# Performance work log

Hardware: AMD Instinct MI355X
Metric: run time of the kernel (lower is better)

Reference implementation:

```python
import jax, jax.numpy as jnp
import numpy as np
import math

B, S, HID = 2, 2048, 512
NH, NKV, HD = 8, 2, 256
ROT = 64          # partial_rotary_factor 0.25 * head_dim 256
ROPE_THETA = 10000000.0
EPS = 1e-6


def _rms_norm(x, w):
    # zero-centered RMSNorm: x / rms * (1 + w)
    rms = jnp.sqrt(jnp.mean(x * x, axis=-1, keepdims=True) + EPS)
    return x / rms * (1.0 + w)


def _partial_rope(x, cos, sin):
    # x: [B,S,H,HD]; cos/sin: [S, ROT//2]
    xr = x[..., :ROT].reshape(*x.shape[:-1], ROT // 2, 2)
    a, b = xr[..., 0], xr[..., 1]
    c = cos[None, :, None, :]
    s = sin[None, :, None, :]
    rot = jnp.stack([a * c - b * s, a * s + b * c], axis=-1).reshape(*x.shape[:-1], ROT)
    return jnp.concatenate([rot, x[..., ROT:]], axis=-1)


def setup_inputs() -> dict:
    key = jax.random.key(0)
    ks = jax.random.split(key, 6)
    x = jax.random.normal(ks[0], (B, S, HID), dtype=jnp.float32)
    # real RoPE frequencies
    inv_freq = 1.0 / (ROPE_THETA ** (np.arange(0, ROT, 2, dtype=np.float32) / ROT))
    t = np.arange(S, dtype=np.float32)
    angles = np.outer(t, inv_freq)  # [S, ROT//2]
    cos = jnp.asarray(np.cos(angles), dtype=jnp.float32)
    sin = jnp.asarray(np.sin(angles), dtype=jnp.float32)
    # additive causal mask [S,S]
    mask = jnp.where(jnp.tril(jnp.ones((S, S), dtype=bool)), 0.0, -1e9).astype(jnp.float32)
    sc = 0.02
    wq = jax.random.normal(ks[1], (HID, NH * HD), dtype=jnp.float32) * sc
    wk = jax.random.normal(ks[2], (HID, NKV * HD), dtype=jnp.float32) * sc
    wv = jax.random.normal(ks[3], (HID, NKV * HD), dtype=jnp.float32) * sc
    wo = jax.random.normal(ks[4], (NH * HD, HID), dtype=jnp.float32) * sc
    q_norm_w = jnp.zeros((HD,), dtype=jnp.float32)
    k_norm_w = jnp.zeros((HD,), dtype=jnp.float32)
    return {"x": x, "cos": cos, "sin": sin, "mask": mask,
            "wq": wq, "wk": wk, "wv": wv, "wo": wo,
            "q_norm_w": q_norm_w, "k_norm_w": k_norm_w}


def reference(x, cos, sin, mask, wq, wk, wv, wo, q_norm_w, k_norm_w):
    b, s, _ = x.shape
    groups = NH // NKV
    q = (x @ wq).reshape(b, s, NH, HD)
    k = (x @ wk).reshape(b, s, NKV, HD)
    v = (x @ wv).reshape(b, s, NKV, HD)
    q = _partial_rope(_rms_norm(q, q_norm_w), cos, sin)
    k = _partial_rope(_rms_norm(k, k_norm_w), cos, sin)
    # GQA: broadcast kv heads to NH
    k = jnp.repeat(k, groups, axis=2)  # [b,s,NH,HD]
    v = jnp.repeat(v, groups, axis=2)
    scale = math.sqrt(HD)
    scores = jnp.einsum('bqhd,bkhd->bhqk', q, k) / scale
    scores = scores + mask[None, None, :, :]
    attn = jax.nn.softmax(scores, axis=-1)
    out = jnp.einsum('bhqk,bkhd->bqhd', attn, v).reshape(b, s, NH * HD)
    return out @ wo
```

## Files before the change

### kernel.cpp

```cpp
#include <hip/hip_runtime.h>

#define S_LEN 2048
#define NHQ 8
#define NKV 2
#define HD 256
#define KVB 32

typedef __attribute__((ext_vector_type(8))) short bf16x8;
typedef __attribute__((ext_vector_type(4))) short bf16x4;
typedef __attribute__((ext_vector_type(4))) float f32x4;
typedef __attribute__((ext_vector_type(16))) float f32x16;
typedef __attribute__((ext_vector_type(4))) unsigned u32x4;

__device__ __forceinline__ short f2bf(float f) {
    unsigned u = __builtin_bit_cast(unsigned, f);
    u += 0x7FFFu + ((u >> 16) & 1u);
    return (short)(u >> 16);
}
__device__ __forceinline__ float bf2f(short s) {
    unsigned u = ((unsigned)(unsigned short)s) << 16;
    return __builtin_bit_cast(float, u);
}
__device__ __forceinline__ unsigned cvtpk(float a, float b) {
    unsigned r;
    asm("v_cvt_pk_bf16_f32 %0, %1, %2" : "=v"(r) : "v"(a), "v"(b));
    return r;
}
__device__ __forceinline__ void gload16(const short* g, short* l) {
    __builtin_amdgcn_global_load_lds((const __attribute__((address_space(1))) unsigned*)g,
                                     (__attribute__((address_space(3))) unsigned*)l, 16, 0, 0);
}
__device__ __forceinline__ float bperm(int srclane, float v) {
    return __builtin_bit_cast(float,
        __builtin_amdgcn_ds_bpermute(srclane * 4, __builtin_bit_cast(int, v)));
}

__global__ __launch_bounds__(256) void cvt_kernel(const float* __restrict__ in,
                                                  short* __restrict__ out, int n) {
    int i = (blockIdx.x * 256 + threadIdx.x) * 4;
    if (i + 3 < n) {
        float4 f = *(const float4*)(in + i);
        bf16x4 o;
        o[0] = f2bf(f.x); o[1] = f2bf(f.y); o[2] = f2bf(f.z); o[3] = f2bf(f.w);
        *(bf16x4*)(out + i) = o;
    }
}

__global__ __launch_bounds__(256) void wt_kernel(const float* __restrict__ in,
                                                 short* __restrict__ out,
                                                 int K, int N) {
    __shared__ short tile[64][72];
    int n0 = blockIdx.x * 64, k0 = blockIdx.y * 64;
    int t = threadIdx.x;
    #pragma unroll
    for (int i = 0; i < 16; i++) {
        int flat = i * 256 + t; int r = flat >> 6, c = flat & 63;
        tile[r][c] = f2bf(in[(long)(k0 + r) * N + n0 + c]);
    }
    __syncthreads();
    #pragma unroll
    for (int i = 0; i < 16; i++) {
        int flat = i * 256 + t; int r = flat >> 6, c = flat & 63;
        out[(long)(n0 + r) * K + k0 + c] = tile[c][r];
    }
}

template<int BN, int WRITE_BF16>
__global__ __launch_bounds__(256) void gemm_bt(const short* __restrict__ A,
                                               const short* __restrict__ Bt,
                                               void* __restrict__ Cv,
                                               int M, int N, int K) {
    constexpr int NI = BN / 32;
    __shared__ short As[128 * 32];
    __shared__ short Bs[BN * 32];
    const int t = threadIdx.x;
    const int lane = t & 63, w = t >> 6;
    const int lr = lane & 15, lg = lane >> 4;
    const int m0 = blockIdx.y * 128, n0 = blockIdx.x * BN;
    const int wm = (w >> 1) * 64, wn = (w & 1) * (BN / 2);

    f32x4 acc[4][NI];
    #pragma unroll
    for (int i = 0; i < 4; i++)
        #pragma unroll
        for (int j = 0; j < NI; j++) acc[i][j] = (f32x4){0.f, 0.f, 0.f, 0.f};

    for (int k0 = 0; k0 < K; k0 += 32) {
        __syncthreads();
        #pragma unroll
        for (int r = 0; r < 2; r++) {
            int sbase = r * 2048 + w * 512;
            int srow = (sbase + lane * 8) >> 5, scol = (sbase + lane * 8) & 31;
            gload16(A + (long)(m0 + srow) * K + k0 + scol, &As[sbase]);
        }
        #pragma unroll
        for (int r = 0; r < BN / 64; r++) {
            int sbase = r * 2048 + w * 512;
            int srow = (sbase + lane * 8) >> 5, scol = (sbase + lane * 8) & 31;
            gload16(Bt + (long)(n0 + srow) * K + k0 + scol, &Bs[sbase]);
        }
        __syncthreads();
        bf16x8 af[4], bfr[NI];
        #pragma unroll
        for (int mi = 0; mi < 4; mi++)
            af[mi] = *(const bf16x8*)&As[(wm + mi * 16 + lr) * 32 + lg * 8];
        #pragma unroll
        for (int ni = 0; ni < NI; ni++)
            bfr[ni] = *(const bf16x8*)&Bs[(wn + ni * 16 + lr) * 32 + lg * 8];
        #pragma unroll
        for (int mi = 0; mi < 4; mi++)
            #pragma unroll
            for (int ni = 0; ni < NI; ni++)
                acc[mi][ni] = __builtin_amdgcn_mfma_f32_16x16x32_bf16(af[mi], bfr[ni], acc[mi][ni], 0, 0, 0);
    }
    #pragma unroll
    for (int mi = 0; mi < 4; mi++)
    #pragma unroll
    for (int ni = 0; ni < NI; ni++)
    #pragma unroll
    for (int r = 0; r < 4; r++) {
        long row = m0 + wm + mi * 16 + lg * 4 + r;
        long col = n0 + wn + ni * 16 + lr;
        float v = acc[mi][ni][r];
        if (WRITE_BF16) ((short*)Cv)[row * N + col] = f2bf(v);
        else            ((float*)Cv)[row * N + col] = v;
    }
}

__global__ __launch_bounds__(256) void norm_rope_kernel(
    const short* __restrict__ in, short* __restrict__ out,
    const float* __restrict__ w, const float* __restrict__ cosb,
    const float* __restrict__ sinb, int H, long ldin, long cofs,
    long ob, long oh, long os, float scale) {
    int vec = blockIdx.x * 4 + (threadIdx.x >> 6);
    int lane = threadIdx.x & 63;
    int token = vec / H, head = vec % H;
    int b = token / S_LEN, s = token % S_LEN;

    bf16x4 xv = *(const bf16x4*)(in + (long)token * ldin + cofs + head * 256 + lane * 4);
    float x0 = bf2f(xv[0]), x1 = bf2f(xv[1]), x2 = bf2f(xv[2]), x3 = bf2f(xv[3]);
    float ss = x0 * x0 + x1 * x1 + x2 * x2 + x3 * x3;
    #pragma unroll
    for (int m = 1; m < 64; m <<= 1) ss += __shfl_xor(ss, m);
    float inv = rsqrtf(ss * (1.f / 256.f) + 1e-6f);

    float4 wv = *(const float4*)(w + lane * 4);
    float y0 = x0 * inv * (1.f + wv.x);
    float y1 = x1 * inv * (1.f + wv.y);
    float y2 = x2 * inv * (1.f + wv.z);
    float y3 = x3 * inv * (1.f + wv.w);

    if (lane < 16) {
        float2 c = *(const float2*)&cosb[s * 32 + lane * 2];
        float2 sn = *(const float2*)&sinb[s * 32 + lane * 2];
        float a0 = y0 * c.x - y1 * sn.x, b0 = y0 * sn.x + y1 * c.x;
        float a1 = y2 * c.y - y3 * sn.y, b1 = y2 * sn.y + y3 * c.y;
        y0 = a0; y1 = b0; y2 = a1; y3 = b1;
    }
    y0 *= scale; y1 *= scale; y2 *= scale; y3 *= scale;
    long oidx = (long)b * ob + (long)head * oh + (long)s * os + lane * 4;
    bf16x4 o; o[0] = f2bf(y0); o[1] = f2bf(y1); o[2] = f2bf(y2); o[3] = f2bf(y3);
    *(bf16x4*)(out + oidx) = o;
}

__global__ __launch_bounds__(256) void transpose_v_kernel(const short* __restrict__ C,
                                                          short* __restrict__ vr) {
    __shared__ short tile[64][65];
    int s0 = blockIdx.x * 64, d0 = blockIdx.y * 64;
    int bkv = blockIdx.z; int b = bkv >> 1, kv = bkv & 1;
    int t = threadIdx.x;
    #pragma unroll
    for (int i = 0; i < 16; i++) {
        int flat = i * 256 + t; int si = flat >> 6, di = flat & 63;
        tile[si][di] = C[(long)(b * S_LEN + s0 + si) * 3072 + 2560 + kv * 256 + d0 + di];
    }
    __syncthreads();
    #pragma unroll
    for (int i = 0; i < 16; i++) {
        int flat = i * 256 + t; int di = flat >> 6, si = flat & 63;
        vr[(long)(bkv * 256 + d0 + di) * S_LEN + s0 + si] = tile[si][di];
    }
}

__global__ __launch_bounds__(256, 2) void flash_kernel(const short* __restrict__ Q,
                                                       const short* __restrict__ Kt,
                                                       const short* __restrict__ Vt,
                                                       short* __restrict__ O) {
    __shared__ __align__(16) char smem[66048];

    int idx = blockIdx.x;
    int xcd = idx & 7, slot = idx >> 3;
    int bh = xcd * 2 + (slot & 1);
    int j  = 31 - (slot >> 1);
    int h = bh & 7, b = bh >> 3;
    int kv = h >> 2;
    int t = threadIdx.x, lane = t & 63, w = t >> 6;
    int g = w >> 1, p = w & 1;
    int ln = lane & 31, hi = lane >> 5;
    int q0 = j * 64 + g * 32;
    int qg = q0 + ln;

    const short* Kb = Kt + (long)(b * NKV + kv) * S_LEN * HD;
    const short* Vb = Vt + (long)(b * NKV + kv) * HD * S_LEN;

    bf16x8 qf[16];
    {
        const short* qrow = Q + ((long)(b * S_LEN + qg) * NHQ + h) * HD + hi * 8;
        #pragma unroll
        for (int dc = 0; dc < 16; dc++) qf[dc] = *(const bf16x8*)&qrow[dc * 16];
    }

    f32x16 acc[8];
    #pragma unroll
    for (int i = 0; i < 8; i++)
        #pragma unroll
        for (int jj = 0; jj < 16; jj++) acc[i][jj] = 0.f;
    float m = -1e30f, l = 0.f;

    auto stage = [&](int ph2) {
        #pragma unroll
        for (int pp = 0; pp < 2; pp++) {
            int k0s = (2 * ph2 + pp) * KVB;
            short* Ktile = (short*)(smem + pp * 16384);
            short* Vtile = (short*)(smem + 32768 + pp * 16384);
            #pragma unroll
            for (int c = 0; c < 4; c++) {
                int o = c * 4096 + w * 1024 + lane * 16;
                int key = o >> 9, db = o & 511;
                gload16(Kb + (long)(k0s + key) * HD + ((db ^ ((key & 7) << 4)) >> 1),
                        Ktile + (c * 4096 + w * 1024) / 2);
                int d = o >> 6, kb = o & 63;
                gload16(Vb + (long)d * S_LEN + k0s + ((kb ^ ((d & 6) << 3)) >> 1),
                        Vtile + (c * 4096 + w * 1024) / 2);
            }
        }
    };

    auto compute = [&](int k0) {
        const char* Ks = (const char*)smem + p * 16384;
        const char* Vs = (const char*)smem + 32768 + p * 16384;
        f32x16 sA, sB;
        #pragma unroll
        for (int r = 0; r < 16; r++) { sA[r] = 0.f; sB[r] = 0.f; }
        __builtin_amdgcn_s_setprio(1);
        #pragma unroll
        for (int dc = 0; dc < 16; dc += 2) {
            int kb0 = (dc * 32 + hi * 16) ^ ((ln & 7) << 4);
            int kb1 = ((dc + 1) * 32 + hi * 16) ^ ((ln & 7) << 4);
            bf16x8 kf0 = *(const bf16x8*)(Ks + ln * 512 + kb0);
            bf16x8 kf1 = *(const bf16x8*)(Ks + ln * 512 + kb1);
            sA = __builtin_amdgcn_mfma_f32_32x32x16_bf16(kf0, qf[dc],     sA, 0, 0, 0);
            sB = __builtin_amdgcn_mfma_f32_32x32x16_bf16(kf1, qf[dc + 1], sB, 0, 0, 0);
        }
        __builtin_amdgcn_s_setprio(0);
        f32x16 s;
        #pragma unroll
        for (int r = 0; r < 16; r++) s[r] = sA[r] + sB[r];

        if (k0 + KVB - 1 > q0) {
            #pragma unroll
            for (int r = 0; r < 16; r++) {
                int key_g = k0 + (r & 3) + 8 * (r >> 2) + 4 * hi;
                if (key_g > qg) s[r] = -1e30f;
            }
        }
        float mt = s[0];
        #pragma unroll
        for (int r = 1; r < 16; r++) mt = fmaxf(mt, s[r]);
        mt = fmaxf(mt, __shfl_xor(mt, 32));
        float mn = m;
        if (!__all(mt <= m + 8.f)) {
            mn = fmaxf(m, mt);
            float f = __expf(m - mn);
            m = mn;
            float fr[16];
            #pragma unroll
            for (int r = 0; r < 16; r++)
                fr[r] = bperm((r & 3) + 8 * (r >> 2) + 4 * hi, f);
            #pragma unroll
            for (int i = 0; i < 8; i++)
                #pragma unroll
                for (int r = 0; r < 16; r++) acc[i][r] *= fr[r];
            l *= f;
        }
        float pr[16], ps = 0.f;
        #pragma unroll
        for (int r = 0; r < 16; r++) { pr[r] = __expf(s[r] - mn); ps += pr[r]; }
        ps += __shfl_xor(ps, 32);
        l += ps;

        unsigned pw[8];
        #pragma unroll
        for (int kc = 0; kc < 2; kc++) {
            unsigned X = cvtpk(pr[kc * 8 + 0], pr[kc * 8 + 1]);
            unsigned Y = cvtpk(pr[kc * 8 + 4], pr[kc * 8 + 5]);
            unsigned Z = cvtpk(pr[kc * 8 + 2], pr[kc * 8 + 3]);
            unsigned W = cvtpk(pr[kc * 8 + 6], pr[kc * 8 + 7]);
            asm volatile("v_permlane32_swap_b32 %0, %1" : "+v"(X), "+v"(Y));
            asm volatile("v_permlane32_swap_b32 %0, %1" : "+v"(Z), "+v"(W));
            pw[kc * 4 + 0] = X; pw[kc * 4 + 1] = Z;
            pw[kc * 4 + 2] = Y; pw[kc * 4 + 3] = W;
        }
        u32x4 w0v = {pw[0], pw[1], pw[2], pw[3]};
        u32x4 w1v = {pw[4], pw[5], pw[6], pw[7]};
        bf16x8 pa0 = __builtin_bit_cast(bf16x8, w0v);
        bf16x8 pa1 = __builtin_bit_cast(bf16x8, w1v);

        __builtin_amdgcn_s_setprio(1);
        #pragma unroll
        for (int db = 0; db < 8; db++) {
            int drow = db * 32 + ln;
            int sw = (drow & 6) << 3;
            bf16x8 vf0 = *(const bf16x8*)(Vs + drow * 64 + ((hi * 16) ^ sw));
            bf16x8 vf1 = *(const bf16x8*)(Vs + drow * 64 + ((32 + hi * 16) ^ sw));
            acc[db] = __builtin_amdgcn_mfma_f32_32x32x16_bf16(pa0, vf0, acc[db], 0, 0, 0);
            acc[db] = __builtin_amdgcn_mfma_f32_32x32x16_bf16(pa1, vf1, acc[db], 0, 0, 0);
        }
        __builtin_amdgcn_s_setprio(0);
    };

    stage(0);
    for (int ph = 0; ph <= j; ph++) {
        asm volatile("s_waitcnt vmcnt(0)" ::: "memory");
        __builtin_amdgcn_s_barrier();
        int k0 = (2 * ph + p) * KVB;
        if (k0 <= q0 + 31) compute(k0);
        __builtin_amdgcn_s_barrier();
        if (ph < j) stage(ph + 1);
        __builtin_amdgcn_sched_barrier(0);
    }

    float* accb = (float*)smem;
    float* mlb  = (float*)(smem + 65536);
    if (p == 1) {
        #pragma unroll
        for (int db = 0; db < 8; db++)
            #pragma unroll
            for (int r = 0; r < 16; r++)
                accb[g * 8192 + (db * 16 + r) * 64 + hi * 32 + ln] = acc[db][r];
        if (hi == 0) { mlb[g * 32 + ln] = m; mlb[64 + g * 32 + ln] = l; }
    }
    __syncthreads();
    if (p == 0) {
        float m1 = mlb[g * 32 + ln], l1 = mlb[64 + g * 32 + ln];
        float M  = fmaxf(m, m1);
        float f0 = __expf(m - M), f1 = __expf(m1 - M);
        float lt = l * f0 + l1 * f1;
        float w0 = f0 / lt, w1 = f1 / lt;
        float fr0[16], fr1[16];
        #pragma unroll
        for (int r = 0; r < 16; r++) {
            int crow = (r & 3) + 8 * (r >> 2) + 4 * hi;
            fr0[r] = bperm(crow, w0);
            fr1[r] = bperm(crow, w1);
        }
        #pragma unroll
        for (int db = 0; db < 8; db++)
            #pragma unroll
            for (int r = 0; r < 16; r++) {
                float a1 = accb[g * 8192 + (db * 16 + r) * 64 + hi * 32 + ln];
                int qrow = q0 + (r & 3) + 8 * (r >> 2) + 4 * hi;
                O[(long)(b * S_LEN + qrow) * 2048 + h * HD + db * 32 + ln] =
                    f2bf(acc[db][r] * fr0[r] + a1 * fr1[r]);
            }
    }
}

extern "C" void kernel_launch(void* const* d_in, const int* in_sizes, int n_in,
                              void* d_out, int out_size, void* d_ws, size_t ws_size,
                              hipStream_t stream) {
    const float* x    = (const float*)d_in[0];
    const float* cosb = (const float*)d_in[1];
    const float* sinb = (const float*)d_in[2];
    const float* wq   = (const float*)d_in[4];
    const float* wk   = (const float*)d_in[5];
    const float* wv   = (const float*)d_in[6];
    const float* wo   = (const float*)d_in[7];
    const float* qnw  = (const float*)d_in[8];
    const float* knw  = (const float*)d_in[9];
    float* out = (float*)d_out;

    char* ws = (char*)d_ws;
    short* xb   = (short*)(ws + 0);
    short* wfus = (short*)(ws + 4194304);
    short* wot  = (short*)(ws + 7340032);
    short* C    = (short*)(ws + 9437184);
    short* ao   = (short*)(ws + 9437184);
    short* qro  = (short*)(ws + 34603008);
    short* kr   = (short*)(ws + 51380224);
    short* vr   = (short*)(ws + 55574528);

    cvt_kernel<<<2048, 256, 0, stream>>>(x, xb, 2097152);
    wt_kernel<<<dim3(32, 8), 256, 0, stream>>>(wq, wfus,              512, 2048);
    wt_kernel<<<dim3(8, 8),  256, 0, stream>>>(wk, wfus + 2048 * 512, 512, 512);
    wt_kernel<<<dim3(8, 8),  256, 0, stream>>>(wv, wfus + 2560 * 512, 512, 512);
    wt_kernel<<<dim3(8, 32), 256, 0, stream>>>(wo, wot, 2048, 512);

    gemm_bt<128, 1><<<dim3(24, 32), 256, 0, stream>>>(xb, wfus, C, 4096, 3072, 512);

    norm_rope_kernel<<<8192, 256, 0, stream>>>(C, qro, qnw, cosb, sinb, 8,
                                               3072L, 0L, 4194304L, 256L, 2048L, 0.0625f);
    norm_rope_kernel<<<2048, 256, 0, stream>>>(C, kr, knw, cosb, sinb, 2,
                                               3072L, 2048L, 1048576L, 524288L, 256L, 1.0f);
    transpose_v_kernel<<<dim3(32, 4, 4), 256, 0, stream>>>(C, vr);

    flash_kernel<<<512, 256, 0, stream>>>(qro, kr, vr, ao);

    gemm_bt<64, 0><<<dim3(8, 32), 256, 0, stream>>>(ao, wot, out, 4096, 512, 2048);
}
```

Measured before the change: 199.9 us.

## Fuse Q norm+RoPE into flash kernel and split K/V staging pipeline

Removes the separate Q RMSNorm+RoPE kernel. The flash kernel now reads raw Q from the fused projection output and applies the norm, rotary and scale in registers while the first K/V tiles load. The K and V loads are split into separate stages with partial vmcnt waits, so the next K tile loads during softmax and PV, and V loads during the next QK. The block-to-tile mapping is also changed to pair long and short causal rows across the two grid halves. This adds barriers per iteration and more register pressure.

```diff
diff --git a/kernel.cpp b/kernel.cpp
--- a/kernel.cpp
+++ b/kernel.cpp
@@ -182,16 +182,21 @@
     }
 }
 
-__global__ __launch_bounds__(256, 2) void flash_kernel(const short* __restrict__ Q,
+__global__ __launch_bounds__(256, 2) void flash_kernel(const short* __restrict__ Cq,
                                                        const short* __restrict__ Kt,
                                                        const short* __restrict__ Vt,
-                                                       short* __restrict__ O) {
+                                                       short* __restrict__ O,
+                                                       const float* __restrict__ qnw,
+                                                       const float* __restrict__ cosb,
+                                                       const float* __restrict__ sinb) {
     __shared__ __align__(16) char smem[66048];
 
     int idx = blockIdx.x;
-    int xcd = idx & 7, slot = idx >> 3;
+    int half = idx >> 8, rm = idx & 255;
+    int xcd = rm & 7, slot = rm >> 3;
     int bh = xcd * 2 + (slot & 1);
-    int j  = 31 - (slot >> 1);
+    int jj = slot >> 1;
+    int j  = half ? jj : (31 - jj);
     int h = bh & 7, b = bh >> 3;
     int kv = h >> 2;
     int t = threadIdx.x, lane = t & 63, w = t >> 6;
@@ -203,32 +208,28 @@
     const short* Kb = Kt + (long)(b * NKV + kv) * S_LEN * HD;
     const short* Vb = Vt + (long)(b * NKV + kv) * HD * S_LEN;
 
-    bf16x8 qf[16];
-    {
-        const short* qrow = Q + ((long)(b * S_LEN + qg) * NHQ + h) * HD + hi * 8;
-        #pragma unroll
-        for (int dc = 0; dc < 16; dc++) qf[dc] = *(const bf16x8*)&qrow[dc * 16];
-    }
-
-    f32x16 acc[8];
-    #pragma unroll
-    for (int i = 0; i < 8; i++)
-        #pragma unroll
-        for (int jj = 0; jj < 16; jj++) acc[i][jj] = 0.f;
-    float m = -1e30f, l = 0.f;
-
-    auto stage = [&](int ph2) {
+    auto stageK = [&](int ph2) {
         #pragma unroll
         for (int pp = 0; pp < 2; pp++) {
             int k0s = (2 * ph2 + pp) * KVB;
             short* Ktile = (short*)(smem + pp * 16384);
-            short* Vtile = (short*)(smem + 32768 + pp * 16384);
             #pragma unroll
             for (int c = 0; c < 4; c++) {
                 int o = c * 4096 + w * 1024 + lane * 16;
                 int key = o >> 9, db = o & 511;
                 gload16(Kb + (long)(k0s + key) * HD + ((db ^ ((key & 7) << 4)) >> 1),
                         Ktile + (c * 4096 + w * 1024) / 2);
+            }
+        }
+    };
+    auto stageV = [&](int ph2) {
+        #pragma unroll
+        for (int pp = 0; pp < 2; pp++) {
+            int k0s = (2 * ph2 + pp) * KVB;
+            short* Vtile = (short*)(smem + 32768 + pp * 16384);
+            #pragma unroll
+            for (int c = 0; c < 4; c++) {
+                int o = c * 4096 + w * 1024 + lane * 16;
                 int d = o >> 6, kb = o & 63;
                 gload16(Vb + (long)d * S_LEN + k0s + ((kb ^ ((d & 6) << 3)) >> 1),
                         Vtile + (c * 4096 + w * 1024) / 2);
@@ -236,98 +237,159 @@
         }
     };
 
-    auto compute = [&](int k0) {
-        const char* Ks = (const char*)smem + p * 16384;
-        const char* Vs = (const char*)smem + 32768 + p * 16384;
-        f32x16 sA, sB;
-        #pragma unroll
-        for (int r = 0; r < 16; r++) { sA[r] = 0.f; sB[r] = 0.f; }
-        __builtin_amdgcn_s_setprio(1);
-        #pragma unroll
-        for (int dc = 0; dc < 16; dc += 2) {
-            int kb0 = (dc * 32 + hi * 16) ^ ((ln & 7) << 4);
-            int kb1 = ((dc + 1) * 32 + hi * 16) ^ ((ln & 7) << 4);
-            bf16x8 kf0 = *(const bf16x8*)(Ks + ln * 512 + kb0);
-            bf16x8 kf1 = *(const bf16x8*)(Ks + ln * 512 + kb1);
-            sA = __builtin_amdgcn_mfma_f32_32x32x16_bf16(kf0, qf[dc],     sA, 0, 0, 0);
-            sB = __builtin_amdgcn_mfma_f32_32x32x16_bf16(kf1, qf[dc + 1], sB, 0, 0, 0);
-        }
-        __builtin_amdgcn_s_setprio(0);
-        f32x16 s;
-        #pragma unroll
-        for (int r = 0; r < 16; r++) s[r] = sA[r] + sB[r];
-
-        if (k0 + KVB - 1 > q0) {
-            #pragma unroll
-            for (int r = 0; r < 16; r++) {
-                int key_g = k0 + (r & 3) + 8 * (r >> 2) + 4 * hi;
-                if (key_g > qg) s[r] = -1e30f;
-            }
-        }
-        float mt = s[0];
-        #pragma unroll
-        for (int r = 1; r < 16; r++) mt = fmaxf(mt, s[r]);
-        mt = fmaxf(mt, __shfl_xor(mt, 32));
-        float mn = m;
-        if (!__all(mt <= m + 8.f)) {
-            mn = fmaxf(m, mt);
-            float f = __expf(m - mn);
-            m = mn;
-            float fr[16];
-            #pragma unroll
-            for (int r = 0; r < 16; r++)
-                fr[r] = bperm((r & 3) + 8 * (r >> 2) + 4 * hi, f);
-            #pragma unroll
-            for (int i = 0; i < 8; i++)
-                #pragma unroll
-                for (int r = 0; r < 16; r++) acc[i][r] *= fr[r];
-            l *= f;
-        }
-        float pr[16], ps = 0.f;
-        #pragma unroll
-        for (int r = 0; r < 16; r++) { pr[r] = __expf(s[r] - mn); ps += pr[r]; }
-        ps += __shfl_xor(ps, 32);
-        l += ps;
-
-        unsigned pw[8];
-        #pragma unroll
-        for (int kc = 0; kc < 2; kc++) {
-            unsigned X = cvtpk(pr[kc * 8 + 0], pr[kc * 8 + 1]);
-            unsigned Y = cvtpk(pr[kc * 8 + 4], pr[kc * 8 + 5]);
-            unsigned Z = cvtpk(pr[kc * 8 + 2], pr[kc * 8 + 3]);
-            unsigned W = cvtpk(pr[kc * 8 + 6], pr[kc * 8 + 7]);
-            asm volatile("v_permlane32_swap_b32 %0, %1" : "+v"(X), "+v"(Y));
-            asm volatile("v_permlane32_swap_b32 %0, %1" : "+v"(Z), "+v"(W));
-            pw[kc * 4 + 0] = X; pw[kc * 4 + 1] = Z;
-            pw[kc * 4 + 2] = Y; pw[kc * 4 + 3] = W;
-        }
-        u32x4 w0v = {pw[0], pw[1], pw[2], pw[3]};
-        u32x4 w1v = {pw[4], pw[5], pw[6], pw[7]};
-        bf16x8 pa0 = __builtin_bit_cast(bf16x8, w0v);
-        bf16x8 pa1 = __builtin_bit_cast(bf16x8, w1v);
-
-        __builtin_amdgcn_s_setprio(1);
-        #pragma unroll
-        for (int db = 0; db < 8; db++) {
-            int drow = db * 32 + ln;
-            int sw = (drow & 6) << 3;
-            bf16x8 vf0 = *(const bf16x8*)(Vs + drow * 64 + ((hi * 16) ^ sw));
-            bf16x8 vf1 = *(const bf16x8*)(Vs + drow * 64 + ((32 + hi * 16) ^ sw));
-            acc[db] = __builtin_amdgcn_mfma_f32_32x32x16_bf16(pa0, vf0, acc[db], 0, 0, 0);
-            acc[db] = __builtin_amdgcn_mfma_f32_32x32x16_bf16(pa1, vf1, acc[db], 0, 0, 0);
-        }
-        __builtin_amdgcn_s_setprio(0);
-    };
-
-    stage(0);
+    stageK(0); stageV(0);
+
+    bf16x8 qf[16];
+    {
+        const short* qrow = Cq + (long)(b * S_LEN + qg) * 3072 + h * 256 + hi * 8;
+        #pragma unroll
+        for (int dc = 0; dc < 16; dc++) qf[dc] = *(const bf16x8*)&qrow[dc * 16];
+        float ss = 0.f;
+        #pragma unroll
+        for (int dc = 0; dc < 16; dc++)
+            #pragma unroll
+            for (int e = 0; e < 8; e++) { float v = bf2f(qf[dc][e]); ss += v * v; }
+        ss += __shfl_xor(ss, 32);
+        float inv = rsqrtf(ss * (1.f / 256.f) + 1e-6f);
+        #pragma unroll
+        for (int dc = 0; dc < 16; dc++) {
+            float y[8];
+            float4 w0 = *(const float4*)&qnw[dc * 16 + hi * 8];
+            float4 w1 = *(const float4*)&qnw[dc * 16 + hi * 8 + 4];
+            y[0] = bf2f(qf[dc][0]) * inv * (1.f + w0.x);
+            y[1] = bf2f(qf[dc][1]) * inv * (1.f + w0.y);
+            y[2] = bf2f(qf[dc][2]) * inv * (1.f + w0.z);
+            y[3] = bf2f(qf[dc][3]) * inv * (1.f + w0.w);
+            y[4] = bf2f(qf[dc][4]) * inv * (1.f + w1.x);
+            y[5] = bf2f(qf[dc][5]) * inv * (1.f + w1.y);
+            y[6] = bf2f(qf[dc][6]) * inv * (1.f + w1.z);
+            y[7] = bf2f(qf[dc][7]) * inv * (1.f + w1.w);
+            if (dc < 4) {
+                float4 c4 = *(const float4*)&cosb[qg * 32 + dc * 8 + hi * 4];
+                float4 s4 = *(const float4*)&sinb[qg * 32 + dc * 8 + hi * 4];
+                float a, bb;
+                a = y[0]; bb = y[1]; y[0] = a * c4.x - bb * s4.x; y[1] = a * s4.x + bb * c4.x;
+                a = y[2]; bb = y[3]; y[2] = a * c4.y - bb * s4.y; y[3] = a * s4.y + bb * c4.y;
+                a = y[4]; bb = y[5]; y[4] = a * c4.z - bb * s4.z; y[5] = a * s4.z + bb * c4.z;
+                a = y[6]; bb = y[7]; y[6] = a * c4.w - bb * s4.w; y[7] = a * s4.w + bb * c4.w;
+            }
+            bf16x8 o;
+            #pragma unroll
+            for (int e = 0; e < 8; e++) o[e] = f2bf(y[e] * 0.0625f);
+            qf[dc] = o;
+        }
+    }
+
+    f32x16 acc[8];
+    #pragma unroll
+    for (int i = 0; i < 8; i++)
+        #pragma unroll
+        for (int r = 0; r < 16; r++) acc[i][r] = 0.f;
+    float m = -1e30f, l = 0.f;
+
     for (int ph = 0; ph <= j; ph++) {
-        asm volatile("s_waitcnt vmcnt(0)" ::: "memory");
+        const bool last = (ph == j);
+        asm volatile("s_waitcnt vmcnt(8)" ::: "memory");
         __builtin_amdgcn_s_barrier();
         int k0 = (2 * ph + p) * KVB;
-        if (k0 <= q0 + 31) compute(k0);
+        bool act = (k0 <= q0 + 31);
+
+        f32x16 s;
+        if (act) {
+            const char* Ks = (const char*)smem + p * 16384;
+            f32x16 sA, sB;
+            #pragma unroll
+            for (int r = 0; r < 16; r++) { sA[r] = 0.f; sB[r] = 0.f; }
+            __builtin_amdgcn_s_setprio(1);
+            #pragma unroll
+            for (int dc = 0; dc < 16; dc += 2) {
+                int kb0 = (dc * 32 + hi * 16) ^ ((ln & 7) << 4);
+                int kb1 = ((dc + 1) * 32 + hi * 16) ^ ((ln & 7) << 4);
+                bf16x8 kf0 = *(const bf16x8*)(Ks + ln * 512 + kb0);
+                bf16x8 kf1 = *(const bf16x8*)(Ks + ln * 512 + kb1);
+                sA = __builtin_amdgcn_mfma_f32_32x32x16_bf16(kf0, qf[dc],     sA, 0, 0, 0);
+                sB = __builtin_amdgcn_mfma_f32_32x32x16_bf16(kf1, qf[dc + 1], sB, 0, 0, 0);
+            }
+            __builtin_amdgcn_s_setprio(0);
+            #pragma unroll
+            for (int r = 0; r < 16; r++) s[r] = sA[r] + sB[r];
+        }
         __builtin_amdgcn_s_barrier();
-        if (ph < j) stage(ph + 1);
+        if (!last) stageK(ph + 1);
         __builtin_amdgcn_sched_barrier(0);
+
+        bf16x8 pa0, pa1;
+        if (act) {
+            if (k0 + KVB - 1 > q0) {
+                #pragma unroll
+                for (int r = 0; r < 16; r++) {
+                    int key_g = k0 + (r & 3) + 8 * (r >> 2) + 4 * hi;
+                    if (key_g > qg) s[r] = -1e30f;
+                }
+            }
+            float mt = s[0];
+            #pragma unroll
+            for (int r = 1; r < 16; r++) mt = fmaxf(mt, s[r]);
+            mt = fmaxf(mt, __shfl_xor(mt, 32));
+            float mn = m;
+            if (!__all(mt <= m + 8.f)) {
+                mn = fmaxf(m, mt);
+                float f = __expf(m - mn);
+                m = mn;
+                float fr[16];
+                #pragma unroll
+                for (int r = 0; r < 16; r++)
+                    fr[r] = bperm((r & 3) + 8 * (r >> 2) + 4 * hi, f);
+                #pragma unroll
+                for (int i = 0; i < 8; i++)
+                    #pragma unroll
+                    for (int r = 0; r < 16; r++) acc[i][r] *= fr[r];
+                l *= f;
+            }
+            float pr[16], ps = 0.f;
+            #pragma unroll
+            for (int r = 0; r < 16; r++) { pr[r] = __expf(s[r] - mn); ps += pr[r]; }
+            ps += __shfl_xor(ps, 32);
+            l += ps;
+
+            unsigned pw[8];
+            #pragma unroll
+            for (int kc = 0; kc < 2; kc++) {
+                unsigned X = cvtpk(pr[kc * 8 + 0], pr[kc * 8 + 1]);
+                unsigned Y = cvtpk(pr[kc * 8 + 4], pr[kc * 8 + 5]);
+                unsigned Z = cvtpk(pr[kc * 8 + 2], pr[kc * 8 + 3]);
+                unsigned W = cvtpk(pr[kc * 8 + 6], pr[kc * 8 + 7]);
+                asm volatile("v_permlane32_swap_b32 %0, %1" : "+v"(X), "+v"(Y));
+                asm volatile("v_permlane32_swap_b32 %0, %1" : "+v"(Z), "+v"(W));
+                pw[kc * 4 + 0] = X; pw[kc * 4 + 1] = Z;
+                pw[kc * 4 + 2] = Y; pw[kc * 4 + 3] = W;
+            }
+            u32x4 w0v = {pw[0], pw[1], pw[2], pw[3]};
+            u32x4 w1v = {pw[4], pw[5], pw[6], pw[7]};
+            pa0 = __builtin_bit_cast(bf16x8, w0v);
+            pa1 = __builtin_bit_cast(bf16x8, w1v);
+        }
+
+        if (last) { asm volatile("s_waitcnt vmcnt(0)" ::: "memory"); }
+        else      { asm volatile("s_waitcnt vmcnt(8)" ::: "memory"); }
+        __builtin_amdgcn_s_barrier();
+
+        if (act) {
+            const char* Vs = (const char*)smem + 32768 + p * 16384;
+            __builtin_amdgcn_s_setprio(1);
+            #pragma unroll
+            for (int db = 0; db < 8; db++) {
+                int drow = db * 32 + ln;
+                int sw = (drow & 6) << 3;
+                bf16x8 vf0 = *(const bf16x8*)(Vs + drow * 64 + ((hi * 16) ^ sw));
+                bf16x8 vf1 = *(const bf16x8*)(Vs + drow * 64 + ((32 + hi * 16) ^ sw));
+                acc[db] = __builtin_amdgcn_mfma_f32_32x32x16_bf16(pa0, vf0, acc[db], 0, 0, 0);
+                acc[db] = __builtin_amdgcn_mfma_f32_32x32x16_bf16(pa1, vf1, acc[db], 0, 0, 0);
+            }
+            __builtin_amdgcn_s_setprio(0);
+        }
+        __builtin_amdgcn_s_barrier();
+        if (!last) stageV(ph + 1);
     }
 
     float* accb = (float*)smem;
@@ -385,8 +447,7 @@
     short* wfus = (short*)(ws + 4194304);
     short* wot  = (short*)(ws + 7340032);
     short* C    = (short*)(ws + 9437184);
-    short* ao   = (short*)(ws + 9437184);
-    short* qro  = (short*)(ws + 34603008);
+    short* ao   = (short*)(ws + 34603008);
     short* kr   = (short*)(ws + 51380224);
     short* vr   = (short*)(ws + 55574528);
 
@@ -398,13 +459,11 @@
 
     gemm_bt<128, 1><<<dim3(24, 32), 256, 0, stream>>>(xb, wfus, C, 4096, 3072, 512);
 
-    norm_rope_kernel<<<8192, 256, 0, stream>>>(C, qro, qnw, cosb, sinb, 8,
-                                               3072L, 0L, 4194304L, 256L, 2048L, 0.0625f);
     norm_rope_kernel<<<2048, 256, 0, stream>>>(C, kr, knw, cosb, sinb, 2,
                                                3072L, 2048L, 1048576L, 524288L, 256L, 1.0f);
     transpose_v_kernel<<<dim3(32, 4, 4), 256, 0, stream>>>(C, vr);
 
-    flash_kernel<<<512, 256, 0, stream>>>(qro, kr, vr, ao);
+    flash_kernel<<<512, 256, 0, stream>>>(C, kr, vr, ao, qnw, cosb, sinb);
 
     gemm_bt<64, 0><<<dim3(8, 32), 256, 0, stream>>>(ao, wot, out, 4096, 512, 2048);
 }
```

Measured after the change: 201.8 us. Within noise of the previous version (+0.9%).

## Split K and V staging to overlap next-tile loads with softmax and PV

Applied to the files above, without the earlier changes.

Separates the shared-memory staging of K and V tiles so the next K tile is loaded right after QK^T, while softmax and PV run, and the next V tile is loaded after PV. Waits become partial (vmcnt(8)) instead of draining all loads, and Q fragment loads are issued after the first stage is launched. The aim is to hide global-load latency behind compute, at the cost of an extra barrier per iteration and reliance on a precise in-flight load count.

```diff
diff --git a/kernel.cpp b/kernel.cpp
--- a/kernel.cpp
+++ b/kernel.cpp
@@ -203,32 +203,28 @@
     const short* Kb = Kt + (long)(b * NKV + kv) * S_LEN * HD;
     const short* Vb = Vt + (long)(b * NKV + kv) * HD * S_LEN;
 
-    bf16x8 qf[16];
-    {
-        const short* qrow = Q + ((long)(b * S_LEN + qg) * NHQ + h) * HD + hi * 8;
-        #pragma unroll
-        for (int dc = 0; dc < 16; dc++) qf[dc] = *(const bf16x8*)&qrow[dc * 16];
-    }
-
-    f32x16 acc[8];
-    #pragma unroll
-    for (int i = 0; i < 8; i++)
-        #pragma unroll
-        for (int jj = 0; jj < 16; jj++) acc[i][jj] = 0.f;
-    float m = -1e30f, l = 0.f;
-
-    auto stage = [&](int ph2) {
+    auto stageK = [&](int ph2) {
         #pragma unroll
         for (int pp = 0; pp < 2; pp++) {
             int k0s = (2 * ph2 + pp) * KVB;
             short* Ktile = (short*)(smem + pp * 16384);
-            short* Vtile = (short*)(smem + 32768 + pp * 16384);
             #pragma unroll
             for (int c = 0; c < 4; c++) {
                 int o = c * 4096 + w * 1024 + lane * 16;
                 int key = o >> 9, db = o & 511;
                 gload16(Kb + (long)(k0s + key) * HD + ((db ^ ((key & 7) << 4)) >> 1),
                         Ktile + (c * 4096 + w * 1024) / 2);
+            }
+        }
+    };
+    auto stageV = [&](int ph2) {
+        #pragma unroll
+        for (int pp = 0; pp < 2; pp++) {
+            int k0s = (2 * ph2 + pp) * KVB;
+            short* Vtile = (short*)(smem + 32768 + pp * 16384);
+            #pragma unroll
+            for (int c = 0; c < 4; c++) {
+                int o = c * 4096 + w * 1024 + lane * 16;
                 int d = o >> 6, kb = o & 63;
                 gload16(Vb + (long)d * S_LEN + k0s + ((kb ^ ((d & 6) << 3)) >> 1),
                         Vtile + (c * 4096 + w * 1024) / 2);
@@ -236,98 +232,125 @@
         }
     };
 
-    auto compute = [&](int k0) {
-        const char* Ks = (const char*)smem + p * 16384;
-        const char* Vs = (const char*)smem + 32768 + p * 16384;
-        f32x16 sA, sB;
-        #pragma unroll
-        for (int r = 0; r < 16; r++) { sA[r] = 0.f; sB[r] = 0.f; }
-        __builtin_amdgcn_s_setprio(1);
-        #pragma unroll
-        for (int dc = 0; dc < 16; dc += 2) {
-            int kb0 = (dc * 32 + hi * 16) ^ ((ln & 7) << 4);
-            int kb1 = ((dc + 1) * 32 + hi * 16) ^ ((ln & 7) << 4);
-            bf16x8 kf0 = *(const bf16x8*)(Ks + ln * 512 + kb0);
-            bf16x8 kf1 = *(const bf16x8*)(Ks + ln * 512 + kb1);
-            sA = __builtin_amdgcn_mfma_f32_32x32x16_bf16(kf0, qf[dc],     sA, 0, 0, 0);
-            sB = __builtin_amdgcn_mfma_f32_32x32x16_bf16(kf1, qf[dc + 1], sB, 0, 0, 0);
-        }
-        __builtin_amdgcn_s_setprio(0);
-        f32x16 s;
-        #pragma unroll
-        for (int r = 0; r < 16; r++) s[r] = sA[r] + sB[r];
-
-        if (k0 + KVB - 1 > q0) {
-            #pragma unroll
-            for (int r = 0; r < 16; r++) {
-                int key_g = k0 + (r & 3) + 8 * (r >> 2) + 4 * hi;
-                if (key_g > qg) s[r] = -1e30f;
-            }
-        }
-        float mt = s[0];
-        #pragma unroll
-        for (int r = 1; r < 16; r++) mt = fmaxf(mt, s[r]);
-        mt = fmaxf(mt, __shfl_xor(mt, 32));
-        float mn = m;
-        if (!__all(mt <= m + 8.f)) {
-            mn = fmaxf(m, mt);
-            float f = __expf(m - mn);
-            m = mn;
-            float fr[16];
-            #pragma unroll
-            for (int r = 0; r < 16; r++)
-                fr[r] = bperm((r & 3) + 8 * (r >> 2) + 4 * hi, f);
-            #pragma unroll
-            for (int i = 0; i < 8; i++)
-                #pragma unroll
-                for (int r = 0; r < 16; r++) acc[i][r] *= fr[r];
-            l *= f;
-        }
-        float pr[16], ps = 0.f;
-        #pragma unroll
-        for (int r = 0; r < 16; r++) { pr[r] = __expf(s[r] - mn); ps += pr[r]; }
-        ps += __shfl_xor(ps, 32);
-        l += ps;
-
-        unsigned pw[8];
-        #pragma unroll
-        for (int kc = 0; kc < 2; kc++) {
-            unsigned X = cvtpk(pr[kc * 8 + 0], pr[kc * 8 + 1]);
-            unsigned Y = cvtpk(pr[kc * 8 + 4], pr[kc * 8 + 5]);
-            unsigned Z = cvtpk(pr[kc * 8 + 2], pr[kc * 8 + 3]);
-            unsigned W = cvtpk(pr[kc * 8 + 6], pr[kc * 8 + 7]);
-            asm volatile("v_permlane32_swap_b32 %0, %1" : "+v"(X), "+v"(Y));
-            asm volatile("v_permlane32_swap_b32 %0, %1" : "+v"(Z), "+v"(W));
-            pw[kc * 4 + 0] = X; pw[kc * 4 + 1] = Z;
-            pw[kc * 4 + 2] = Y; pw[kc * 4 + 3] = W;
-        }
-        u32x4 w0v = {pw[0], pw[1], pw[2], pw[3]};
-        u32x4 w1v = {pw[4], pw[5], pw[6], pw[7]};
-        bf16x8 pa0 = __builtin_bit_cast(bf16x8, w0v);
-        bf16x8 pa1 = __builtin_bit_cast(bf16x8, w1v);
-
-        __builtin_amdgcn_s_setprio(1);
-        #pragma unroll
-        for (int db = 0; db < 8; db++) {
-            int drow = db * 32 + ln;
-            int sw = (drow & 6) << 3;
-            bf16x8 vf0 = *(const bf16x8*)(Vs + drow * 64 + ((hi * 16) ^ sw));
-            bf16x8 vf1 = *(const bf16x8*)(Vs + drow * 64 + ((32 + hi * 16) ^ sw));
-            acc[db] = __builtin_amdgcn_mfma_f32_32x32x16_bf16(pa0, vf0, acc[db], 0, 0, 0);
-            acc[db] = __builtin_amdgcn_mfma_f32_32x32x16_bf16(pa1, vf1, acc[db], 0, 0, 0);
-        }
-        __builtin_amdgcn_s_setprio(0);
-    };
-
-    stage(0);
+    stageK(0); stageV(0);
+
+    bf16x8 qf[16];
+    {
+        const short* qrow = Q + ((long)(b * S_LEN + qg) * NHQ + h) * HD + hi * 8;
+        #pragma unroll
+        for (int dc = 0; dc < 16; dc++) qf[dc] = *(const bf16x8*)&qrow[dc * 16];
+    }
+
+    f32x16 acc[8];
+    #pragma unroll
+    for (int i = 0; i < 8; i++)
+        #pragma unroll
+        for (int r = 0; r < 16; r++) acc[i][r] = 0.f;
+    float m = -1e30f, l = 0.f;
+
     for (int ph = 0; ph <= j; ph++) {
-        asm volatile("s_waitcnt vmcnt(0)" ::: "memory");
+        const bool last = (ph == j);
+        asm volatile("s_waitcnt vmcnt(8)" ::: "memory");
         __builtin_amdgcn_s_barrier();
         int k0 = (2 * ph + p) * KVB;
-        if (k0 <= q0 + 31) compute(k0);
+        bool act = (k0 <= q0 + 31);
+
+        f32x16 s;
+        if (act) {
+            const char* Ks = (const char*)smem + p * 16384;
+            f32x16 sA, sB;
+            #pragma unroll
+            for (int r = 0; r < 16; r++) { sA[r] = 0.f; sB[r] = 0.f; }
+            __builtin_amdgcn_s_setprio(1);
+            #pragma unroll
+            for (int dc = 0; dc < 16; dc += 2) {
+                int kb0 = (dc * 32 + hi * 16) ^ ((ln & 7) << 4);
+                int kb1 = ((dc + 1) * 32 + hi * 16) ^ ((ln & 7) << 4);
+                bf16x8 kf0 = *(const bf16x8*)(Ks + ln * 512 + kb0);
+                bf16x8 kf1 = *(const bf16x8*)(Ks + ln * 512 + kb1);
+                sA = __builtin_amdgcn_mfma_f32_32x32x16_bf16(kf0, qf[dc],     sA, 0, 0, 0);
+                sB = __builtin_amdgcn_mfma_f32_32x32x16_bf16(kf1, qf[dc + 1], sB, 0, 0, 0);
+            }
+            __builtin_amdgcn_s_setprio(0);
+            #pragma unroll
+            for (int r = 0; r < 16; r++) s[r] = sA[r] + sB[r];
+        }
         __builtin_amdgcn_s_barrier();
-        if (ph < j) stage(ph + 1);
+        if (!last) stageK(ph + 1);
         __builtin_amdgcn_sched_barrier(0);
+
+        bf16x8 pa0, pa1;
+        if (act) {
+            if (k0 + KVB - 1 > q0) {
+                #pragma unroll
+                for (int r = 0; r < 16; r++) {
+                    int key_g = k0 + (r & 3) + 8 * (r >> 2) + 4 * hi;
+                    if (key_g > qg) s[r] = -1e30f;
+                }
+            }
+            float mt = s[0];
+            #pragma unroll
+            for (int r = 1; r < 16; r++) mt = fmaxf(mt, s[r]);
+            mt = fmaxf(mt, __shfl_xor(mt, 32));
+            float mn = m;
+            if (!__all(mt <= m + 8.f)) {
+                mn = fmaxf(m, mt);
+                float f = __expf(m - mn);
+                m = mn;
+                float fr[16];
+                #pragma unroll
+                for (int r = 0; r < 16; r++)
+                    fr[r] = bperm((r & 3) + 8 * (r >> 2) + 4 * hi, f);
+                #pragma unroll
+                for (int i = 0; i < 8; i++)
+                    #pragma unroll
+                    for (int r = 0; r < 16; r++) acc[i][r] *= fr[r];
+                l *= f;
+            }
+            float pr[16], ps = 0.f;
+            #pragma unroll
+            for (int r = 0; r < 16; r++) { pr[r] = __expf(s[r] - mn); ps += pr[r]; }
+            ps += __shfl_xor(ps, 32);
+            l += ps;
+
+            unsigned pw[8];
+            #pragma unroll
+            for (int kc = 0; kc < 2; kc++) {
+                unsigned X = cvtpk(pr[kc * 8 + 0], pr[kc * 8 + 1]);
+                unsigned Y = cvtpk(pr[kc * 8 + 4], pr[kc * 8 + 5]);
+                unsigned Z = cvtpk(pr[kc * 8 + 2], pr[kc * 8 + 3]);
+                unsigned W = cvtpk(pr[kc * 8 + 6], pr[kc * 8 + 7]);
+                asm volatile("v_permlane32_swap_b32 %0, %1" : "+v"(X), "+v"(Y));
+                asm volatile("v_permlane32_swap_b32 %0, %1" : "+v"(Z), "+v"(W));
+                pw[kc * 4 + 0] = X; pw[kc * 4 + 1] = Z;
+                pw[kc * 4 + 2] = Y; pw[kc * 4 + 3] = W;
+            }
+            u32x4 w0v = {pw[0], pw[1], pw[2], pw[3]};
+            u32x4 w1v = {pw[4], pw[5], pw[6], pw[7]};
+            pa0 = __builtin_bit_cast(bf16x8, w0v);
+            pa1 = __builtin_bit_cast(bf16x8, w1v);
+        }
+
+        if (last) { asm volatile("s_waitcnt vmcnt(0)" ::: "memory"); }
+        else      { asm volatile("s_waitcnt vmcnt(8)" ::: "memory"); }
+        __builtin_amdgcn_s_barrier();
+
+        if (act) {
+            const char* Vs = (const char*)smem + 32768 + p * 16384;
+            __builtin_amdgcn_s_setprio(1);
+            #pragma unroll
+            for (int db = 0; db < 8; db++) {
+                int drow = db * 32 + ln;
+                int sw = (drow & 6) << 3;
+                bf16x8 vf0 = *(const bf16x8*)(Vs + drow * 64 + ((hi * 16) ^ sw));
+                bf16x8 vf1 = *(const bf16x8*)(Vs + drow * 64 + ((32 + hi * 16) ^ sw));
+                acc[db] = __builtin_amdgcn_mfma_f32_32x32x16_bf16(pa0, vf0, acc[db], 0, 0, 0);
+                acc[db] = __builtin_amdgcn_mfma_f32_32x32x16_bf16(pa1, vf1, acc[db], 0, 0, 0);
+            }
+            __builtin_amdgcn_s_setprio(0);
+        }
+        __builtin_amdgcn_s_barrier();
+        if (!last) stageV(ph + 1);
     }
 
     float* accb = (float*)smem;
```

New measurement: 208.3 us. 4.2% more time.
